# Performance work log

Measured on AMD Instinct MI355X. Metric: run time of the kernel, lower is better.

## Reference

```python
import jax, jax.numpy as jnp
import numpy as np

B, T, N = 8, 4096, 1024
N_KNOWN = 768  # known (sampled) nodes; unknown = N - N_KNOWN = 256
DENSITY = 0.03


def setup_inputs() -> dict:
    key = jax.random.key(0)
    k1, k2, k3, k4 = jax.random.split(key, 4)
    x = jax.random.normal(k1, (B, T, N), dtype=jnp.float32)
    # binary adjacency with ~DENSITY edges; add identity so every node has >=1 neighbor
    A = (jax.random.uniform(k2, (N, N)) < DENSITY).astype(jnp.float32)
    A = jnp.maximum(A, jnp.eye(N, dtype=jnp.float32))
    # unknown = complement(sample, N): 256 distinct node ids, ascending (set-iteration order)
    perm = jax.random.permutation(k3, N)
    unknown = jnp.sort(perm[N_KNOWN:]).astype(jnp.int32)
    # mask = scalar mean of matrix.values[:, sample] in the original module
    mask = jax.random.uniform(k4, (), dtype=jnp.float32)
    return {"input": x, "A": A, "unknown": unknown, "mask": mask}


def reference(input, A, unknown, mask):
    # 1) overwrite unknown columns with the scalar mask (in-place in the original)
    x = input.at[:, :, unknown].set(mask)
    deg = jnp.sum(A, axis=1)  # [N] neighbor counts (A is binary)
    # 2) sequential in-place per-node neighbor mean: later unknown nodes see
    #    the already-updated values of earlier ones, so order matters -> lax.scan.
    def step(x, node):
        # mean over neighbors == masked weighted sum via the binary adjacency row
        val = jnp.einsum('btn,n->bt', x, A[node]) / deg[node]  # [B, T]
        return x.at[:, :, node].set(val), None
    x, _ = jax.lax.scan(step, x, unknown)
    return x
```

## Files before the change

kernel.cpp:

```cpp
#include <hip/hip_runtime.h>

#define U 256
#define NN 1024
#define NROWS 32768
#define LCAP 32
#define DUMMY 256

typedef __bf16 bf16_t;
typedef __bf16 bf16x4 __attribute__((ext_vector_type(4)));
typedef __bf16 bf16x8 __attribute__((ext_vector_type(8)));
typedef float f32x4 __attribute__((ext_vector_type(4)));
typedef unsigned short u16;
typedef unsigned short u16x8 __attribute__((ext_vector_type(8)));
typedef short s16x4 __attribute__((ext_vector_type(4)));

__global__ __launch_bounds__(256) void k_struct(const float* __restrict__ A,
    const int* __restrict__ unknown, const float* __restrict__ maskp,
    float* __restrict__ invDeg, float* __restrict__ coef,
    int* __restrict__ lessCnt, u16* __restrict__ lessIdx,
    int* __restrict__ uflag, short* __restrict__ pmap)
{
    __shared__ int sunk[U];
    __shared__ float sdeg;
    __shared__ int scnt, sge;
    int t = threadIdx.x, k = blockIdx.x;
    sunk[t] = unknown[t];
    if (t == 0) { sdeg = 0.f; scnt = 0; sge = 0; }
    __syncthreads();
    int uk = sunk[k];
    float dsum = 0.f;
    for (int i = 0; i < NN / 256; ++i) {
        int n = t + 256 * i;
        float a = A[(size_t)uk * NN + n];
        if (a != 0.f) {
            dsum += a;
            int lo = 0, hi = U;
            while (lo < hi) { int mid = (lo + hi) >> 1; if (sunk[mid] < n) lo = mid + 1; else hi = mid; }
            if (lo < U && sunk[lo] == n) {
                if (lo < k) {
                    int id = atomicAdd(&scnt, 1);
                    if (id < LCAP) lessIdx[k * LCAP + id] = (u16)lo;
                } else {
                    atomicAdd(&sge, 1);
                }
            }
        }
    }
    atomicAdd(&sdeg, dsum);
    __syncthreads();
    int c0 = min(scnt, LCAP);
    if (t >= c0 && t < LCAP) lessIdx[k * LCAP + t] = DUMMY;
    if (t == 0) {
        float inv = 1.f / sdeg;
        invDeg[k] = inv;
        coef[k] = (float)sge * maskp[0] * inv;
        lessCnt[k] = c0;
    }
    if (k == 0) {
        for (int i = 0; i < NN / 256; ++i) { uflag[t + 256 * i] = 0; pmap[t + 256 * i] = -1; }
        __syncthreads();
        uflag[sunk[t]] = 1;
        pmap[sunk[t]] = (short)t;
    }
}

__global__ __launch_bounds__(256) void k_levels(const int* __restrict__ lessCnt,
    const u16* __restrict__ lessIdx, int* __restrict__ order,
    int* __restrict__ levelStart, int* __restrict__ nLevOut)
{
    __shared__ u16 sIdx[U * LCAP];
    __shared__ int slvl[U];
    __shared__ int sc[U];
    __shared__ int hist[U];
    __shared__ int changed;
    int t = threadIdx.x;
    for (int i = t; i < U * LCAP / 2; i += 256) ((unsigned int*)sIdx)[i] = ((const unsigned int*)lessIdx)[i];
    sc[t] = lessCnt[t];
    slvl[t] = 0; hist[t] = 0;
    __syncthreads();
    for (int iter = 0; iter < U; ++iter) {
        if (t == 0) changed = 0;
        __syncthreads();
        int c = sc[t], nl = 0;
        for (int i = 0; i < c; ++i) nl = max(nl, slvl[sIdx[t * LCAP + i]] + 1);
        if (nl > slvl[t]) { slvl[t] = nl; changed = 1; }
        __syncthreads();
        if (!changed) break;
    }
    int L = slvl[t];
    atomicAdd(&hist[L], 1);
    __syncthreads();
    if (t == 0) {
        int acc = 0, lastl = 0;
        for (int l = 0; l < U; ++l) {
            int h = hist[l];
            hist[l] = acc;
            acc += h;
            if (h > 0) lastl = l;
        }
        nLevOut[0] = lastl + 1;
    }
    __syncthreads();
    levelStart[t] = hist[t];
    if (t == 0) levelStart[U] = U;
    __syncthreads();
    int pos = atomicAdd(&hist[L], 1);
    order[pos] = t;
}

__global__ __launch_bounds__(256) void k_mbuild(const int* __restrict__ lessCnt,
    const u16* __restrict__ lessIdx, const float* __restrict__ invDeg,
    const int* __restrict__ order, const int* __restrict__ levelStart,
    const int* __restrict__ nLevp, float* __restrict__ MT)
{
    __shared__ float Ms[(U + 1) * 32];
    __shared__ u16 sIdx[U * LCAP];
    __shared__ float sInv[U];
    __shared__ u16 sOrd[U];
    __shared__ unsigned char sCnt[U];
    __shared__ int sLs[U + 1];
    int t = threadIdx.x;
    int g = t >> 5, c = t & 31;
    int col = blockIdx.x * 32 + c;
    for (int i = t; i < U * LCAP / 2; i += 256) ((unsigned int*)sIdx)[i] = ((const unsigned int*)lessIdx)[i];
    sInv[t] = invDeg[t];
    sOrd[t] = (u16)order[t];
    sCnt[t] = (unsigned char)lessCnt[t];
    sLs[t] = levelStart[t];
    if (t == 0) sLs[U] = levelStart[U];
    if (t < 32) Ms[U * 32 + t] = 0.f;
    int nLev = nLevp[0];
    __syncthreads();
    for (int lev = 0; lev < nLev; ++lev) {
        int s = sLs[lev], e = sLs[lev + 1];
        for (int base = s + g; base < e; base += 8) {
            int k = sOrd[base];
            int cnt = sCnt[k];
            const u16* ip = &sIdx[k * LCAP];
            float sum = 0.f;
            for (int b = 0; b < cnt; b += 8) {
                u16x8 jv = *(const u16x8*)(ip + b);
                float v0 = Ms[jv[0] * 32 + c];
                float v1 = Ms[jv[1] * 32 + c];
                float v2 = Ms[jv[2] * 32 + c];
                float v3 = Ms[jv[3] * 32 + c];
                float v4 = Ms[jv[4] * 32 + c];
                float v5 = Ms[jv[5] * 32 + c];
                float v6 = Ms[jv[6] * 32 + c];
                float v7 = Ms[jv[7] * 32 + c];
                sum += ((v0 + v1) + (v2 + v3)) + ((v4 + v5) + (v6 + v7));
            }
            float m = (k == col ? 1.f : 0.f) + sInv[k] * sum;
            Ms[k * 32 + c] = m;
            MT[(size_t)col * U + k] = m;
        }
        __syncthreads();
    }
}

__global__ __launch_bounds__(256) void k_wbuild(const float* __restrict__ A,
    const int* __restrict__ unknown, const float* __restrict__ invDeg,
    const float* __restrict__ coef, const int* __restrict__ uflag,
    const float* __restrict__ MT, bf16_t* __restrict__ Wb, float* __restrict__ bvec)
{
    int t = threadIdx.x, d = blockIdx.x;
    if (d == NN) {
        __shared__ float scf[U];
        scf[t] = coef[t];
        __syncthreads();
        float s = 0.f;
        #pragma unroll 8
        for (int c = 0; c < U; ++c) s += MT[(size_t)c * U + t] * scf[c];
        bvec[t] = s;
        return;
    }
    if (uflag[d]) { Wb[(size_t)t * NN + d] = (bf16_t)0.f; return; }
    __shared__ int nnz;
    __shared__ int cs[64];
    __shared__ float vsv[64];
    if (t == 0) nnz = 0;
    __syncthreads();
    float a = A[(size_t)unknown[t] * NN + d];
    if (a != 0.f) {
        int id = atomicAdd(&nnz, 1);
        if (id < 64) { cs[id] = t; vsv[id] = a * invDeg[t]; }
    }
    __syncthreads();
    int n = min(nnz, 64);
    float s = 0.f;
    for (int i = 0; i < n; ++i)
        s += MT[(size_t)cs[i] * U + t] * vsv[i];
    Wb[(size_t)t * NN + d] = (bf16_t)s;
}

#define RT 32
#define BK 64
#define LDX 72
#define URS 257

__global__ __launch_bounds__(256) void k_main(const float* __restrict__ x,
    const short* __restrict__ pmap, const bf16_t* __restrict__ Wb,
    const float* __restrict__ bvec, float* __restrict__ out)
{
    __shared__ __align__(16) char smem[41472];
    __shared__ float sb[U];
    __shared__ short spm[NN];
    bf16_t* Xl = (bf16_t*)smem;
    bf16_t* Vl = (bf16_t*)(smem + 4608);
    float* Ures = (float*)smem;
    int t = threadIdx.x;
    int w = t >> 6, l = t & 63;
    int m = l & 15, q = l >> 4;
    size_t row0 = (size_t)blockIdx.x * RT;
    sb[t] = bvec[t];
    #pragma unroll
    for (int j = 0; j < 4; ++j) spm[t + 256 * j] = pmap[t + 256 * j];
    f32x4 acc[2][4] = {};
    int uv = t >> 3, du = (t & 7) * 8;
    for (int db = 0; db < NN; db += BK) {
        __syncthreads();
        #pragma unroll
        for (int ii = 0; ii < 2; ++ii) {
            int flat = t + ii * 256;
            int r = flat >> 4, c4 = (flat & 15) * 4;
            float4 v = *(const float4*)(x + (row0 + r) * NN + db + c4);
            bf16x4 hv = { (bf16_t)v.x, (bf16_t)v.y, (bf16_t)v.z, (bf16_t)v.w };
            *(bf16x4*)(&Xl[r * LDX + c4]) = hv;
        }
        #pragma unroll
        for (int i = 0; i < 8; ++i) {
            int u = uv + 32 * i;
            *(bf16x8*)(&Vl[u * LDX + du]) = *(const bf16x8*)(Wb + (size_t)u * NN + db + du);
        }
        __syncthreads();
        #pragma unroll
        for (int s = 0; s < 2; ++s) {
            bf16x8 af[2];
            #pragma unroll
            for (int R = 0; R < 2; ++R)
                af[R] = *(bf16x8*)(&Xl[(R * 16 + m) * LDX + s * 32 + q * 8]);
            #pragma unroll
            for (int T = 0; T < 4; ++T) {
                bf16x8 bfr = *(bf16x8*)(&Vl[((w * 4 + T) * 16 + m) * LDX + s * 32 + q * 8]);
                #pragma unroll
                for (int R = 0; R < 2; ++R)
                    acc[R][T] = __builtin_amdgcn_mfma_f32_16x16x32_bf16(af[R], bfr, acc[R][T], 0, 0, 0);
            }
        }
    }
    __syncthreads();
    #pragma unroll
    for (int R = 0; R < 2; ++R) {
        #pragma unroll
        for (int T = 0; T < 4; ++T) {
            int u = (w * 4 + T) * 16 + m;
            float bb = sb[u];
            #pragma unroll
            for (int i = 0; i < 4; ++i)
                Ures[(R * 16 + q * 4 + i) * URS + u] = acc[R][T][i] + bb;
        }
    }
    __syncthreads();
    s16x4 pm = *(const s16x4*)(&spm[t * 4]);
    #pragma unroll 4
    for (int i = 0; i < RT; ++i) {
        float4 v = *(const float4*)(x + (row0 + i) * NN + t * 4);
        if (pm[0] >= 0) v.x = Ures[i * URS + pm[0]];
        if (pm[1] >= 0) v.y = Ures[i * URS + pm[1]];
        if (pm[2] >= 0) v.z = Ures[i * URS + pm[2]];
        if (pm[3] >= 0) v.w = Ures[i * URS + pm[3]];
        *(float4*)(out + (row0 + i) * NN + t * 4) = v;
    }
}

extern "C" void kernel_launch(void* const* d_in, const int* in_sizes, int n_in,
                              void* d_out, int out_size, void* d_ws, size_t ws_size,
                              hipStream_t stream)
{
    const float* x       = (const float*)d_in[0];
    const float* A       = (const float*)d_in[1];
    const int*   unknown = (const int*)d_in[2];
    const float* maskp   = (const float*)d_in[3];
    float* out = (float*)d_out;

    char* ws = (char*)d_ws;
    float*  MT        = (float*)(ws + 0);
    bf16_t* Wb        = (bf16_t*)(ws + 262144);
    float*  invDeg    = (float*)(ws + 786432);
    float*  coef      = (float*)(ws + 787456);
    float*  bvec      = (float*)(ws + 788480);
    int*    lessCnt   = (int*)(ws + 789504);
    u16*    lessIdx   = (u16*)(ws + 790528);
    int*    uflag     = (int*)(ws + 806912);
    short*  pmap      = (short*)(ws + 811008);
    int*    order     = (int*)(ws + 813056);
    int*    levelStart= (int*)(ws + 814080);
    int*    nLev      = (int*)(ws + 815120);

    hipLaunchKernelGGL(k_struct, dim3(U), dim3(256), 0, stream,
                       A, unknown, maskp, invDeg, coef, lessCnt, lessIdx, uflag, pmap);
    hipLaunchKernelGGL(k_levels, dim3(1), dim3(256), 0, stream,
                       lessCnt, lessIdx, order, levelStart, nLev);
    hipLaunchKernelGGL(k_mbuild, dim3(8), dim3(256), 0, stream,
                       lessCnt, lessIdx, invDeg, order, levelStart, nLev, MT);
    hipLaunchKernelGGL(k_wbuild, dim3(NN + 1), dim3(256), 0, stream,
                       A, unknown, invDeg, coef, uflag, MT, Wb, bvec);
    hipLaunchKernelGGL(k_main, dim3(NROWS / RT), dim3(256), 0, stream,
                       x, pmap, Wb, bvec, out);
}
```

Measured before the change: 348.3 us.

## Build W directly by level-wise substitution and stream GEMM operands from global

Replaces the two-step build (the unknown-unknown propagation matrix MT, then W = MT·A) with a single kernel that does forward substitution level by level directly on the W columns and on the bias vector, removing the 256x256 intermediate and one launch. The main GEMM kernel drops its shared-memory staging and loads x and W fragments straight from global into MFMA operands, which removes the barriers but relies on the cache for reuse. The levels kernel keeps each thread's index list in registers and computes maxima in groups of eight. The build kernel has only 17 blocks, which limits parallelism in the setup phase.

```diff
diff --git a/kernel.cpp b/kernel.cpp
--- a/kernel.cpp
+++ b/kernel.cpp
@@ -7,7 +7,6 @@
 #define DUMMY 256
 
 typedef __bf16 bf16_t;
-typedef __bf16 bf16x4 __attribute__((ext_vector_type(4)));
 typedef __bf16 bf16x8 __attribute__((ext_vector_type(8)));
 typedef float f32x4 __attribute__((ext_vector_type(4)));
 typedef unsigned short u16;
@@ -69,26 +68,37 @@
     int* __restrict__ levelStart, int* __restrict__ nLevOut)
 {
     __shared__ u16 sIdx[U * LCAP];
-    __shared__ int slvl[U];
-    __shared__ int sc[U];
+    __shared__ int slvl[U + 1];
     __shared__ int hist[U];
     __shared__ int changed;
     int t = threadIdx.x;
-    for (int i = t; i < U * LCAP / 2; i += 256) ((unsigned int*)sIdx)[i] = ((const unsigned int*)lessIdx)[i];
-    sc[t] = lessCnt[t];
+    for (int i = t; i < U * LCAP / 2; i += 256) ((unsigned*)sIdx)[i] = ((const unsigned*)lessIdx)[i];
+    int cnt = lessCnt[t];
     slvl[t] = 0; hist[t] = 0;
-    __syncthreads();
+    if (t == 0) slvl[U] = -1;
+    __syncthreads();
+    u16x8 jv[4];
+    #pragma unroll
+    for (int b = 0; b < 4; ++b) jv[b] = *(const u16x8*)(&sIdx[t * LCAP + b * 8]);
+    int nb = (cnt + 7) >> 3;
+    int lvl = 0;
     for (int iter = 0; iter < U; ++iter) {
         if (t == 0) changed = 0;
         __syncthreads();
-        int c = sc[t], nl = 0;
-        for (int i = 0; i < c; ++i) nl = max(nl, slvl[sIdx[t * LCAP + i]] + 1);
-        if (nl > slvl[t]) { slvl[t] = nl; changed = 1; }
+        int nl = 0;
+        for (int b = 0; b < nb; ++b) {
+            u16x8 j = jv[b];
+            int m0 = max(slvl[j[0]], slvl[j[1]]);
+            int m1 = max(slvl[j[2]], slvl[j[3]]);
+            int m2 = max(slvl[j[4]], slvl[j[5]]);
+            int m3 = max(slvl[j[6]], slvl[j[7]]);
+            nl = max(nl, max(max(m0, m1), max(m2, m3)) + 1);
+        }
+        if (nl > lvl) { lvl = nl; slvl[t] = nl; changed = 1; }
         __syncthreads();
         if (!changed) break;
     }
-    int L = slvl[t];
-    atomicAdd(&hist[L], 1);
+    atomicAdd(&hist[lvl], 1);
     __syncthreads();
     if (t == 0) {
         int acc = 0, lastl = 0;
@@ -104,110 +114,101 @@
     levelStart[t] = hist[t];
     if (t == 0) levelStart[U] = U;
     __syncthreads();
-    int pos = atomicAdd(&hist[L], 1);
+    int pos = atomicAdd(&hist[lvl], 1);
     order[pos] = t;
 }
 
-__global__ __launch_bounds__(256) void k_mbuild(const int* __restrict__ lessCnt,
-    const u16* __restrict__ lessIdx, const float* __restrict__ invDeg,
+__global__ __launch_bounds__(256) void k_wsub(const float* __restrict__ A,
+    const int* __restrict__ unknown, const float* __restrict__ invDeg,
+    const float* __restrict__ coef, const int* __restrict__ uflag,
+    const int* __restrict__ lessCnt, const u16* __restrict__ lessIdx,
     const int* __restrict__ order, const int* __restrict__ levelStart,
-    const int* __restrict__ nLevp, float* __restrict__ MT)
-{
-    __shared__ float Ms[(U + 1) * 32];
+    const int* __restrict__ nLevp, bf16_t* __restrict__ Wb, float* __restrict__ bvec)
+{
+    int t = threadIdx.x;
+    int nLev = nLevp[0];
+    if (blockIdx.x == 16) {
+        __shared__ float sbv[U + 1];
+        __shared__ u16 bIdx[U * LCAP];
+        __shared__ int bLs[U + 1];
+        __shared__ u16 bOrd[U];
+        __shared__ float bcf[U], biv[U];
+        __shared__ unsigned char bCnt[U];
+        for (int i = t; i < U * LCAP / 2; i += 256) ((unsigned*)bIdx)[i] = ((const unsigned*)lessIdx)[i];
+        bcf[t] = coef[t]; biv[t] = invDeg[t];
+        bCnt[t] = (unsigned char)lessCnt[t];
+        bOrd[t] = (u16)order[t];
+        bLs[t] = levelStart[t];
+        if (t == 0) { bLs[U] = levelStart[U]; sbv[U] = 0.f; }
+        __syncthreads();
+        for (int lev = 0; lev < nLev; ++lev) {
+            int s = bLs[lev], e = bLs[lev + 1];
+            int idx = s + t;
+            if (idx < e) {
+                int k = bOrd[idx];
+                int cn = bCnt[k];
+                float sum = 0.f;
+                for (int b = 0; b < cn; b += 8) {
+                    u16x8 j = *(const u16x8*)(&bIdx[k * LCAP + b]);
+                    sum += ((sbv[j[0]] + sbv[j[1]]) + (sbv[j[2]] + sbv[j[3]]))
+                         + ((sbv[j[4]] + sbv[j[5]]) + (sbv[j[6]] + sbv[j[7]]));
+                }
+                sbv[k] = bcf[k] + biv[k] * sum;
+            }
+            __syncthreads();
+        }
+        bvec[t] = sbv[t];
+        return;
+    }
+    __shared__ float Wl[(U + 1) * 64];
     __shared__ u16 sIdx[U * LCAP];
-    __shared__ float sInv[U];
+    __shared__ int sunk[U];
+    __shared__ float siv[U];
     __shared__ u16 sOrd[U];
     __shared__ unsigned char sCnt[U];
     __shared__ int sLs[U + 1];
-    int t = threadIdx.x;
-    int g = t >> 5, c = t & 31;
-    int col = blockIdx.x * 32 + c;
-    for (int i = t; i < U * LCAP / 2; i += 256) ((unsigned int*)sIdx)[i] = ((const unsigned int*)lessIdx)[i];
-    sInv[t] = invDeg[t];
+    int g = t >> 6, c = t & 63;
+    int cb = blockIdx.x * 64;
+    for (int i = t; i < U * LCAP / 2; i += 256) ((unsigned*)sIdx)[i] = ((const unsigned*)lessIdx)[i];
+    sunk[t] = unknown[t];
+    siv[t] = invDeg[t];
     sOrd[t] = (u16)order[t];
     sCnt[t] = (unsigned char)lessCnt[t];
     sLs[t] = levelStart[t];
     if (t == 0) sLs[U] = levelStart[U];
-    if (t < 32) Ms[U * 32 + t] = 0.f;
-    int nLev = nLevp[0];
+    if (t < 64) Wl[U * 64 + t] = 0.f;
+    float kmask = uflag[cb + c] ? 0.f : 1.f;
     __syncthreads();
     for (int lev = 0; lev < nLev; ++lev) {
         int s = sLs[lev], e = sLs[lev + 1];
-        for (int base = s + g; base < e; base += 8) {
-            int k = sOrd[base];
-            int cnt = sCnt[k];
-            const u16* ip = &sIdx[k * LCAP];
+        for (int idx = s + g; idx < e; idx += 4) {
+            int k = sOrd[idx];
+            float av = A[(size_t)sunk[k] * NN + cb + c];
+            int cn = sCnt[k];
             float sum = 0.f;
-            for (int b = 0; b < cnt; b += 8) {
-                u16x8 jv = *(const u16x8*)(ip + b);
-                float v0 = Ms[jv[0] * 32 + c];
-                float v1 = Ms[jv[1] * 32 + c];
-                float v2 = Ms[jv[2] * 32 + c];
-                float v3 = Ms[jv[3] * 32 + c];
-                float v4 = Ms[jv[4] * 32 + c];
-                float v5 = Ms[jv[5] * 32 + c];
-                float v6 = Ms[jv[6] * 32 + c];
-                float v7 = Ms[jv[7] * 32 + c];
-                sum += ((v0 + v1) + (v2 + v3)) + ((v4 + v5) + (v6 + v7));
+            for (int b = 0; b < cn; b += 8) {
+                u16x8 j = *(const u16x8*)(&sIdx[k * LCAP + b]);
+                sum += ((Wl[j[0] * 64 + c] + Wl[j[1] * 64 + c]) + (Wl[j[2] * 64 + c] + Wl[j[3] * 64 + c]))
+                     + ((Wl[j[4] * 64 + c] + Wl[j[5] * 64 + c]) + (Wl[j[6] * 64 + c] + Wl[j[7] * 64 + c]));
             }
-            float m = (k == col ? 1.f : 0.f) + sInv[k] * sum;
-            Ms[k * 32 + c] = m;
-            MT[(size_t)col * U + k] = m;
-        }
-        __syncthreads();
-    }
-}
-
-__global__ __launch_bounds__(256) void k_wbuild(const float* __restrict__ A,
-    const int* __restrict__ unknown, const float* __restrict__ invDeg,
-    const float* __restrict__ coef, const int* __restrict__ uflag,
-    const float* __restrict__ MT, bf16_t* __restrict__ Wb, float* __restrict__ bvec)
-{
-    int t = threadIdx.x, d = blockIdx.x;
-    if (d == NN) {
-        __shared__ float scf[U];
-        scf[t] = coef[t];
-        __syncthreads();
-        float s = 0.f;
-        #pragma unroll 8
-        for (int c = 0; c < U; ++c) s += MT[(size_t)c * U + t] * scf[c];
-        bvec[t] = s;
-        return;
-    }
-    if (uflag[d]) { Wb[(size_t)t * NN + d] = (bf16_t)0.f; return; }
-    __shared__ int nnz;
-    __shared__ int cs[64];
-    __shared__ float vsv[64];
-    if (t == 0) nnz = 0;
-    __syncthreads();
-    float a = A[(size_t)unknown[t] * NN + d];
-    if (a != 0.f) {
-        int id = atomicAdd(&nnz, 1);
-        if (id < 64) { cs[id] = t; vsv[id] = a * invDeg[t]; }
-    }
-    __syncthreads();
-    int n = min(nnz, 64);
-    float s = 0.f;
-    for (int i = 0; i < n; ++i)
-        s += MT[(size_t)cs[i] * U + t] * vsv[i];
-    Wb[(size_t)t * NN + d] = (bf16_t)s;
+            float wv = siv[k] * (av * kmask + sum);
+            Wl[k * 64 + c] = wv;
+            Wb[(size_t)k * NN + cb + c] = (bf16_t)wv;
+        }
+        __syncthreads();
+    }
 }
 
 #define RT 32
-#define BK 64
-#define LDX 72
 #define URS 257
 
 __global__ __launch_bounds__(256) void k_main(const float* __restrict__ x,
     const short* __restrict__ pmap, const bf16_t* __restrict__ Wb,
     const float* __restrict__ bvec, float* __restrict__ out)
 {
-    __shared__ __align__(16) char smem[41472];
+    __shared__ __align__(16) float Ures[RT * URS];
     __shared__ float sb[U];
     __shared__ short spm[NN];
-    bf16_t* Xl = (bf16_t*)smem;
-    bf16_t* Vl = (bf16_t*)(smem + 4608);
-    float* Ures = (float*)smem;
     int t = threadIdx.x;
     int w = t >> 6, l = t & 63;
     int m = l & 15, q = l >> 4;
@@ -216,37 +217,36 @@
     #pragma unroll
     for (int j = 0; j < 4; ++j) spm[t + 256 * j] = pmap[t + 256 * j];
     f32x4 acc[2][4] = {};
-    int uv = t >> 3, du = (t & 7) * 8;
-    for (int db = 0; db < NN; db += BK) {
-        __syncthreads();
-        #pragma unroll
-        for (int ii = 0; ii < 2; ++ii) {
-            int flat = t + ii * 256;
-            int r = flat >> 4, c4 = (flat & 15) * 4;
-            float4 v = *(const float4*)(x + (row0 + r) * NN + db + c4);
-            bf16x4 hv = { (bf16_t)v.x, (bf16_t)v.y, (bf16_t)v.z, (bf16_t)v.w };
-            *(bf16x4*)(&Xl[r * LDX + c4]) = hv;
-        }
-        #pragma unroll
-        for (int i = 0; i < 8; ++i) {
-            int u = uv + 32 * i;
-            *(bf16x8*)(&Vl[u * LDX + du]) = *(const bf16x8*)(Wb + (size_t)u * NN + db + du);
-        }
-        __syncthreads();
-        #pragma unroll
-        for (int s = 0; s < 2; ++s) {
-            bf16x8 af[2];
-            #pragma unroll
-            for (int R = 0; R < 2; ++R)
-                af[R] = *(bf16x8*)(&Xl[(R * 16 + m) * LDX + s * 32 + q * 8]);
-            #pragma unroll
-            for (int T = 0; T < 4; ++T) {
-                bf16x8 bfr = *(bf16x8*)(&Vl[((w * 4 + T) * 16 + m) * LDX + s * 32 + q * 8]);
-                #pragma unroll
-                for (int R = 0; R < 2; ++R)
-                    acc[R][T] = __builtin_amdgcn_mfma_f32_16x16x32_bf16(af[R], bfr, acc[R][T], 0, 0, 0);
-            }
-        }
+    const float* xp0 = x + (row0 + m) * NN + q * 8;
+    const float* xp1 = x + (row0 + 16 + m) * NN + q * 8;
+    const bf16_t* wp0 = Wb + (size_t)((w * 4 + 0) * 16 + m) * NN + q * 8;
+    const bf16_t* wp1 = Wb + (size_t)((w * 4 + 1) * 16 + m) * NN + q * 8;
+    const bf16_t* wp2 = Wb + (size_t)((w * 4 + 2) * 16 + m) * NN + q * 8;
+    const bf16_t* wp3 = Wb + (size_t)((w * 4 + 3) * 16 + m) * NN + q * 8;
+    for (int db = 0; db < NN; db += 32) {
+        bf16x8 af[2];
+        {
+            float4 v0 = *(const float4*)(xp0 + db);
+            float4 v1 = *(const float4*)(xp0 + db + 4);
+            af[0] = bf16x8{(bf16_t)v0.x, (bf16_t)v0.y, (bf16_t)v0.z, (bf16_t)v0.w,
+                           (bf16_t)v1.x, (bf16_t)v1.y, (bf16_t)v1.z, (bf16_t)v1.w};
+            float4 v2 = *(const float4*)(xp1 + db);
+            float4 v3 = *(const float4*)(xp1 + db + 4);
+            af[1] = bf16x8{(bf16_t)v2.x, (bf16_t)v2.y, (bf16_t)v2.z, (bf16_t)v2.w,
+                           (bf16_t)v3.x, (bf16_t)v3.y, (bf16_t)v3.z, (bf16_t)v3.w};
+        }
+        bf16x8 b0 = *(const bf16x8*)(wp0 + db);
+        bf16x8 b1 = *(const bf16x8*)(wp1 + db);
+        bf16x8 b2 = *(const bf16x8*)(wp2 + db);
+        bf16x8 b3 = *(const bf16x8*)(wp3 + db);
+        acc[0][0] = __builtin_amdgcn_mfma_f32_16x16x32_bf16(af[0], b0, acc[0][0], 0, 0, 0);
+        acc[1][0] = __builtin_amdgcn_mfma_f32_16x16x32_bf16(af[1], b0, acc[1][0], 0, 0, 0);
+        acc[0][1] = __builtin_amdgcn_mfma_f32_16x16x32_bf16(af[0], b1, acc[0][1], 0, 0, 0);
+        acc[1][1] = __builtin_amdgcn_mfma_f32_16x16x32_bf16(af[1], b1, acc[1][1], 0, 0, 0);
+        acc[0][2] = __builtin_amdgcn_mfma_f32_16x16x32_bf16(af[0], b2, acc[0][2], 0, 0, 0);
+        acc[1][2] = __builtin_amdgcn_mfma_f32_16x16x32_bf16(af[1], b2, acc[1][2], 0, 0, 0);
+        acc[0][3] = __builtin_amdgcn_mfma_f32_16x16x32_bf16(af[0], b3, acc[0][3], 0, 0, 0);
+        acc[1][3] = __builtin_amdgcn_mfma_f32_16x16x32_bf16(af[1], b3, acc[1][3], 0, 0, 0);
     }
     __syncthreads();
     #pragma unroll
@@ -284,27 +284,25 @@
     float* out = (float*)d_out;
 
     char* ws = (char*)d_ws;
-    float*  MT        = (float*)(ws + 0);
-    bf16_t* Wb        = (bf16_t*)(ws + 262144);
-    float*  invDeg    = (float*)(ws + 786432);
-    float*  coef      = (float*)(ws + 787456);
-    float*  bvec      = (float*)(ws + 788480);
-    int*    lessCnt   = (int*)(ws + 789504);
-    u16*    lessIdx   = (u16*)(ws + 790528);
-    int*    uflag     = (int*)(ws + 806912);
-    short*  pmap      = (short*)(ws + 811008);
-    int*    order     = (int*)(ws + 813056);
-    int*    levelStart= (int*)(ws + 814080);
-    int*    nLev      = (int*)(ws + 815120);
+    bf16_t* Wb        = (bf16_t*)(ws + 0);
+    float*  invDeg    = (float*)(ws + 524288);
+    float*  coef      = (float*)(ws + 525312);
+    float*  bvec      = (float*)(ws + 526336);
+    int*    lessCnt   = (int*)(ws + 527360);
+    u16*    lessIdx   = (u16*)(ws + 528384);
+    int*    uflag     = (int*)(ws + 544768);
+    short*  pmap      = (short*)(ws + 548864);
+    int*    order     = (int*)(ws + 550912);
+    int*    levelStart= (int*)(ws + 551936);
+    int*    nLev      = (int*)(ws + 553984);
 
     hipLaunchKernelGGL(k_struct, dim3(U), dim3(256), 0, stream,
                        A, unknown, maskp, invDeg, coef, lessCnt, lessIdx, uflag, pmap);
     hipLaunchKernelGGL(k_levels, dim3(1), dim3(256), 0, stream,
                        lessCnt, lessIdx, order, levelStart, nLev);
-    hipLaunchKernelGGL(k_mbuild, dim3(8), dim3(256), 0, stream,
-                       lessCnt, lessIdx, invDeg, order, levelStart, nLev, MT);
-    hipLaunchKernelGGL(k_wbuild, dim3(NN + 1), dim3(256), 0, stream,
-                       A, unknown, invDeg, coef, uflag, MT, Wb, bvec);
+    hipLaunchKernelGGL(k_wsub, dim3(17), dim3(256), 0, stream,
+                       A, unknown, invDeg, coef, uflag, lessCnt, lessIdx,
+                       order, levelStart, nLev, Wb, bvec);
     hipLaunchKernelGGL(k_main, dim3(NROWS / RT), dim3(256), 0, stream,
                        x, pmap, Wb, bvec, out);
 }
```

Measured after the change: 467.9 us. 34.3% more time.
